# Kernel optimization log

Measured on AMD Instinct MI355X. Metric: run time of the kernel, lower is better.

## Reference

```python
import jax, jax.numpy as jnp
import numpy as np

N_TERMS = 2048  # zonotope error terms (x[0] center + 2047 generators)
N = 4096        # neurons


def setup_inputs() -> dict:
    key = jax.random.key(0)
    x = jax.random.normal(key, (N_TERMS, N), dtype=jnp.float32)
    return {"x": x}


def reference(x):
    n_terms, n = x.shape
    # interval bounds of the zonotope
    abs_sum = jnp.sum(jnp.abs(x[1:]), axis=0)      # [n]
    upper = x[0] + abs_sum
    lower = x[0] - abs_sum

    cross = (lower * upper) < 0                    # neuron straddles 0
    pos = lower >= 0                               # strictly non-negative
    crossf = cross.astype(x.dtype)
    posf = pos.astype(x.dtype)

    # 'auto' lambda init: upper/(upper-lower) on crossing neurons, 1 on positive,
    # NaN (0/0) replaced by 0.5; lambda is set via .data => constant w.r.t. x.
    denom = upper - lower
    safe = denom != 0
    lam = posf + crossf * jnp.where(safe, upper / jnp.where(safe, denom, 1.0), 0.5)
    lam = jax.lax.stop_gradient(lam)

    delta = jnp.maximum(-lam * lower, (1.0 - lam) * upper)  # [n]

    center = (delta * 0.5 + lam * x[0]) * crossf + x[0] * posf
    gens = x[1:] * (lam * crossf + posf)                    # [n_terms-1, n]

    # Parallel stream-compaction: crossing neuron i gets its own new error row
    # at n_terms + (# crossings before i). Padded to worst case n new rows;
    # non-crossing writes land on distinct (row, col) slots with value 0.
    ci = cross.astype(jnp.int32)
    rows = n_terms + jnp.cumsum(ci) - ci               # exclusive prefix sum
    cols = jnp.arange(n)

    out = jnp.zeros((n_terms + n, n), x.dtype)
    out = out.at[0].set(center)
    out = out.at[1:n_terms].set(gens)
    out = out.at[rows, cols].add((delta * 0.5) * crossf)
    return out
```

## Files before the change

### kernel.cpp

```cpp
#include <hip/hip_runtime.h>

#define N_TERMS 2048
#define NCOL 4096
#define NC4 (NCOL / 4)
#define NCHUNK 128
#define ROWS_PER_CHUNK (N_TERMS / NCHUNK)

__global__ void k_partial_abs(const float* __restrict__ x, float* __restrict__ partial) {
    int col4 = blockIdx.x * blockDim.x + threadIdx.x;
    int chunk = blockIdx.y;
    int r0 = chunk * ROWS_PER_CHUNK;
    int r1 = r0 + ROWS_PER_CHUNK;
    if (r0 == 0) r0 = 1;
    const float4* x4 = (const float4*)x;
    float4 acc = {0.f, 0.f, 0.f, 0.f};
#pragma unroll
    for (int r = r0; r < r1; ++r) {
        float4 v = x4[(long)r * NC4 + col4];
        acc.x += fabsf(v.x);
        acc.y += fabsf(v.y);
        acc.z += fabsf(v.z);
        acc.w += fabsf(v.w);
    }
    ((float4*)partial)[chunk * NC4 + col4] = acc;
}

__global__ void k_stats(const float* __restrict__ x, const float* __restrict__ partial,
                        float* __restrict__ out0, float* __restrict__ scale,
                        float* __restrict__ dhalf, int* __restrict__ crossflag) {
    int c = blockIdx.x * blockDim.x + threadIdx.x;
    float s0 = 0.f, s1 = 0.f, s2 = 0.f, s3 = 0.f;
#pragma unroll 4
    for (int k = 0; k < NCHUNK; k += 4) {
        s0 += partial[(k + 0) * NCOL + c];
        s1 += partial[(k + 1) * NCOL + c];
        s2 += partial[(k + 2) * NCOL + c];
        s3 += partial[(k + 3) * NCOL + c];
    }
    float s = (s0 + s1) + (s2 + s3);
    float x0 = x[c];
    float u = x0 + s;
    float l = x0 - s;
    bool cross = (l * u) < 0.0f;
    bool pos = (l >= 0.0f);
    float denom = u - l;
    float lam = (pos ? 1.0f : 0.0f) +
                (cross ? ((denom != 0.0f) ? u / denom : 0.5f) : 0.0f);
    float delta = fmaxf(-lam * l, (1.0f - lam) * u);
    float crossf = cross ? 1.0f : 0.0f;
    float posf = pos ? 1.0f : 0.0f;
    out0[c] = (delta * 0.5f + lam * x0) * crossf + x0 * posf;
    scale[c] = lam * crossf + posf;
    dhalf[c] = delta * 0.5f * crossf;
    crossflag[c] = cross ? 1 : 0;
}

__global__ void k_prefix(const int* __restrict__ crossflag, int* __restrict__ rowtarget) {
    const int T = 256;
    const int PER = NCOL / T;
    __shared__ int tsum[T];
    int t = threadIdx.x;
    int base = t * PER;
    int ex[PER];
    int run = 0;
#pragma unroll
    for (int i = 0; i < PER; ++i) {
        ex[i] = run;
        run += crossflag[base + i];
    }
    tsum[t] = run;
    __syncthreads();
    for (int off = 1; off < T; off <<= 1) {
        int v = 0;
        if (t >= off) v = tsum[t - off];
        __syncthreads();
        tsum[t] += v;
        __syncthreads();
    }
    int excl = (t == 0) ? 0 : tsum[t - 1];
#pragma unroll
    for (int i = 0; i < PER; ++i) rowtarget[base + i] = N_TERMS + excl + ex[i];
}

__global__ void k_write(const float* __restrict__ x, const float* __restrict__ scale,
                        const float* __restrict__ dhalf, const int* __restrict__ rowtarget,
                        float* __restrict__ out) {
    long gidx = (long)blockIdx.x * blockDim.x + threadIdx.x;
    int row = (int)(gidx >> 10) + 1;
    int col4 = (int)(gidx & 1023);
    const float4* x4 = (const float4*)x;
    float4* o4 = (float4*)out;
    if (row < N_TERMS) {
        float4 v = x4[(long)row * NC4 + col4];
        float4 sc = ((const float4*)scale)[col4];
        v.x *= sc.x; v.y *= sc.y; v.z *= sc.z; v.w *= sc.w;
        o4[(long)row * NC4 + col4] = v;
    } else {
        int4 rt = ((const int4*)rowtarget)[col4];
        float4 dh = ((const float4*)dhalf)[col4];
        float4 v;
        v.x = (rt.x == row) ? dh.x : 0.0f;
        v.y = (rt.y == row) ? dh.y : 0.0f;
        v.z = (rt.z == row) ? dh.z : 0.0f;
        v.w = (rt.w == row) ? dh.w : 0.0f;
        o4[(long)row * NC4 + col4] = v;
    }
}

extern "C" void kernel_launch(void* const* d_in, const int* in_sizes, int n_in,
                              void* d_out, int out_size, void* d_ws, size_t ws_size,
                              hipStream_t stream) {
    const float* x = (const float*)d_in[0];
    float* out = (float*)d_out;

    float* ws = (float*)d_ws;
    float* partial   = ws;
    float* scale     = partial + NCHUNK * NCOL;
    float* dhalf     = scale + NCOL;
    int*   crossflag = (int*)(dhalf + NCOL);
    int*   rowtarget = crossflag + NCOL;

    k_partial_abs<<<dim3(NC4 / 256, NCHUNK), 256, 0, stream>>>(x, partial);
    k_stats<<<NCOL / 256, 256, 0, stream>>>(x, partial, out, scale, dhalf, crossflag);
    k_prefix<<<1, 256, 0, stream>>>(crossflag, rowtarget);

    const long total4 = (long)(N_TERMS + NCOL - 1) * NC4;
    const int blocks = (int)((total4 + 255) / 256);
    k_write<<<blocks, 256, 0, stream>>>(x, scale, dhalf, rowtarget, out);
}
```

Measured before the change: 140.6 us.

## Fuse four kernels into one cooperative persistent kernel with grid syncs

Merges the partial abs-sum, stats, prefix-scan and write kernels into one cooperative kernel of 512 blocks, separating the phases with grid-wide syncs instead of separate launches. The goal is to remove the launch gaps between the four kernels. In exchange, the final write phase becomes a grid-stride loop over fewer resident blocks. The stats and prefix phases now leave most blocks idle at a grid barrier, and each grid.sync carries its own cost.

```diff
diff --git a/kernel.cpp b/kernel.cpp
--- a/kernel.cpp
+++ b/kernel.cpp
@@ -1,109 +1,126 @@
 #include <hip/hip_runtime.h>
+#include <hip/hip_cooperative_groups.h>
+
+namespace cg = cooperative_groups;
 
 #define N_TERMS 2048
 #define NCOL 4096
-#define NC4 (NCOL / 4)
+#define NC4 1024
 #define NCHUNK 128
-#define ROWS_PER_CHUNK (N_TERMS / NCHUNK)
+#define RPC (N_TERMS / NCHUNK)
+#define NBLK 512
+#define NTHR 256
 
-__global__ void k_partial_abs(const float* __restrict__ x, float* __restrict__ partial) {
-    int col4 = blockIdx.x * blockDim.x + threadIdx.x;
-    int chunk = blockIdx.y;
-    int r0 = chunk * ROWS_PER_CHUNK;
-    int r1 = r0 + ROWS_PER_CHUNK;
-    if (r0 == 0) r0 = 1;
+__global__ void __launch_bounds__(NTHR, 2)
+k_fused(const float* __restrict__ x, float* __restrict__ out, float* __restrict__ ws) {
+    float* partial   = ws;
+    float* scale     = partial + NCHUNK * NCOL;
+    float* dhalf     = scale + NCOL;
+    int*   crossflag = (int*)(dhalf + NCOL);
+    int*   rowtarget = crossflag + NCOL;
+
+    cg::grid_group grid = cg::this_grid();
+    const int b = blockIdx.x;
+    const int t = threadIdx.x;
     const float4* x4 = (const float4*)x;
-    float4 acc = {0.f, 0.f, 0.f, 0.f};
+
+    {
+        int chunk = b >> 2;
+        int col4  = (b & 3) * NTHR + t;
+        int r0 = chunk * RPC;
+        int r1 = r0 + RPC;
+        if (r0 == 0) r0 = 1;
+        float4 acc = {0.f, 0.f, 0.f, 0.f};
 #pragma unroll
-    for (int r = r0; r < r1; ++r) {
-        float4 v = x4[(long)r * NC4 + col4];
-        acc.x += fabsf(v.x);
-        acc.y += fabsf(v.y);
-        acc.z += fabsf(v.z);
-        acc.w += fabsf(v.w);
+        for (int r = r0; r < r1; ++r) {
+            float4 v = x4[(long)r * NC4 + col4];
+            acc.x += fabsf(v.x);
+            acc.y += fabsf(v.y);
+            acc.z += fabsf(v.z);
+            acc.w += fabsf(v.w);
+        }
+        ((float4*)partial)[chunk * NC4 + col4] = acc;
     }
-    ((float4*)partial)[chunk * NC4 + col4] = acc;
-}
+    __threadfence();
+    grid.sync();
 
-__global__ void k_stats(const float* __restrict__ x, const float* __restrict__ partial,
-                        float* __restrict__ out0, float* __restrict__ scale,
-                        float* __restrict__ dhalf, int* __restrict__ crossflag) {
-    int c = blockIdx.x * blockDim.x + threadIdx.x;
-    float s0 = 0.f, s1 = 0.f, s2 = 0.f, s3 = 0.f;
+    if (b < 16) {
+        int c = b * NTHR + t;
+        float s0 = 0.f, s1 = 0.f, s2 = 0.f, s3 = 0.f;
 #pragma unroll 4
-    for (int k = 0; k < NCHUNK; k += 4) {
-        s0 += partial[(k + 0) * NCOL + c];
-        s1 += partial[(k + 1) * NCOL + c];
-        s2 += partial[(k + 2) * NCOL + c];
-        s3 += partial[(k + 3) * NCOL + c];
+        for (int k = 0; k < NCHUNK; k += 4) {
+            s0 += partial[(k + 0) * NCOL + c];
+            s1 += partial[(k + 1) * NCOL + c];
+            s2 += partial[(k + 2) * NCOL + c];
+            s3 += partial[(k + 3) * NCOL + c];
+        }
+        float s = (s0 + s1) + (s2 + s3);
+        float x0 = x[c];
+        float u = x0 + s;
+        float l = x0 - s;
+        bool cross = (l * u) < 0.0f;
+        bool pos = (l >= 0.0f);
+        float denom = u - l;
+        float lam = (pos ? 1.0f : 0.0f) +
+                    (cross ? ((denom != 0.0f) ? u / denom : 0.5f) : 0.0f);
+        float delta = fmaxf(-lam * l, (1.0f - lam) * u);
+        float crossf = cross ? 1.0f : 0.0f;
+        float posf = pos ? 1.0f : 0.0f;
+        out[c] = (delta * 0.5f + lam * x0) * crossf + x0 * posf;
+        scale[c] = lam * crossf + posf;
+        dhalf[c] = delta * 0.5f * crossf;
+        crossflag[c] = cross ? 1 : 0;
     }
-    float s = (s0 + s1) + (s2 + s3);
-    float x0 = x[c];
-    float u = x0 + s;
-    float l = x0 - s;
-    bool cross = (l * u) < 0.0f;
-    bool pos = (l >= 0.0f);
-    float denom = u - l;
-    float lam = (pos ? 1.0f : 0.0f) +
-                (cross ? ((denom != 0.0f) ? u / denom : 0.5f) : 0.0f);
-    float delta = fmaxf(-lam * l, (1.0f - lam) * u);
-    float crossf = cross ? 1.0f : 0.0f;
-    float posf = pos ? 1.0f : 0.0f;
-    out0[c] = (delta * 0.5f + lam * x0) * crossf + x0 * posf;
-    scale[c] = lam * crossf + posf;
-    dhalf[c] = delta * 0.5f * crossf;
-    crossflag[c] = cross ? 1 : 0;
-}
+    __threadfence();
+    grid.sync();
 
-__global__ void k_prefix(const int* __restrict__ crossflag, int* __restrict__ rowtarget) {
-    const int T = 256;
-    const int PER = NCOL / T;
-    __shared__ int tsum[T];
-    int t = threadIdx.x;
-    int base = t * PER;
-    int ex[PER];
-    int run = 0;
+    __shared__ int tsum[NTHR];
+    if (b == 0) {
+        const int PER = NCOL / NTHR;
+        int base = t * PER;
+        int ex[PER];
+        int run = 0;
 #pragma unroll
-    for (int i = 0; i < PER; ++i) {
-        ex[i] = run;
-        run += crossflag[base + i];
+        for (int i = 0; i < PER; ++i) {
+            ex[i] = run;
+            run += crossflag[base + i];
+        }
+        tsum[t] = run;
+        __syncthreads();
+        for (int off = 1; off < NTHR; off <<= 1) {
+            int v = 0;
+            if (t >= off) v = tsum[t - off];
+            __syncthreads();
+            tsum[t] += v;
+            __syncthreads();
+        }
+        int excl = (t == 0) ? 0 : tsum[t - 1];
+#pragma unroll
+        for (int i = 0; i < PER; ++i) rowtarget[base + i] = N_TERMS + excl + ex[i];
     }
-    tsum[t] = run;
-    __syncthreads();
-    for (int off = 1; off < T; off <<= 1) {
-        int v = 0;
-        if (t >= off) v = tsum[t - off];
-        __syncthreads();
-        tsum[t] += v;
-        __syncthreads();
-    }
-    int excl = (t == 0) ? 0 : tsum[t - 1];
-#pragma unroll
-    for (int i = 0; i < PER; ++i) rowtarget[base + i] = N_TERMS + excl + ex[i];
-}
+    __threadfence();
+    grid.sync();
 
-__global__ void k_write(const float* __restrict__ x, const float* __restrict__ scale,
-                        const float* __restrict__ dhalf, const int* __restrict__ rowtarget,
-                        float* __restrict__ out) {
-    long gidx = (long)blockIdx.x * blockDim.x + threadIdx.x;
-    int row = (int)(gidx >> 10) + 1;
-    int col4 = (int)(gidx & 1023);
-    const float4* x4 = (const float4*)x;
+    const long total4 = (long)(N_TERMS + NCOL - 1) * NC4;
     float4* o4 = (float4*)out;
-    if (row < N_TERMS) {
-        float4 v = x4[(long)row * NC4 + col4];
-        float4 sc = ((const float4*)scale)[col4];
-        v.x *= sc.x; v.y *= sc.y; v.z *= sc.z; v.w *= sc.w;
-        o4[(long)row * NC4 + col4] = v;
-    } else {
-        int4 rt = ((const int4*)rowtarget)[col4];
-        float4 dh = ((const float4*)dhalf)[col4];
-        float4 v;
-        v.x = (rt.x == row) ? dh.x : 0.0f;
-        v.y = (rt.y == row) ? dh.y : 0.0f;
-        v.z = (rt.z == row) ? dh.z : 0.0f;
-        v.w = (rt.w == row) ? dh.w : 0.0f;
-        o4[(long)row * NC4 + col4] = v;
+    for (long g = (long)b * NTHR + t; g < total4; g += (long)NBLK * NTHR) {
+        int row  = (int)(g >> 10) + 1;
+        int col4 = (int)(g & 1023);
+        if (row < N_TERMS) {
+            float4 v = x4[(long)row * NC4 + col4];
+            float4 sc = ((const float4*)scale)[col4];
+            v.x *= sc.x; v.y *= sc.y; v.z *= sc.z; v.w *= sc.w;
+            o4[(long)row * NC4 + col4] = v;
+        } else {
+            int4 rt = ((const int4*)rowtarget)[col4];
+            float4 dh = ((const float4*)dhalf)[col4];
+            float4 v;
+            v.x = (rt.x == row) ? dh.x : 0.0f;
+            v.y = (rt.y == row) ? dh.y : 0.0f;
+            v.z = (rt.z == row) ? dh.z : 0.0f;
+            v.w = (rt.w == row) ? dh.w : 0.0f;
+            o4[(long)row * NC4 + col4] = v;
+        }
     }
 }
 
@@ -112,19 +129,9 @@
                               hipStream_t stream) {
     const float* x = (const float*)d_in[0];
     float* out = (float*)d_out;
+    float* ws = (float*)d_ws;
 
-    float* ws = (float*)d_ws;
-    float* partial   = ws;
-    float* scale     = partial + NCHUNK * NCOL;
-    float* dhalf     = scale + NCOL;
-    int*   crossflag = (int*)(dhalf + NCOL);
-    int*   rowtarget = crossflag + NCOL;
-
-    k_partial_abs<<<dim3(NC4 / 256, NCHUNK), 256, 0, stream>>>(x, partial);
-    k_stats<<<NCOL / 256, 256, 0, stream>>>(x, partial, out, scale, dhalf, crossflag);
-    k_prefix<<<1, 256, 0, stream>>>(crossflag, rowtarget);
-
-    const long total4 = (long)(N_TERMS + NCOL - 1) * NC4;
-    const int blocks = (int)((total4 + 255) / 256);
-    k_write<<<blocks, 256, 0, stream>>>(x, scale, dhalf, rowtarget, out);
+    void* args[] = {(void*)&x, (void*)&out, (void*)&ws};
+    hipLaunchCooperativeKernel((const void*)k_fused, dim3(NBLK), dim3(NTHR),
+                               args, 0, stream);
 }
```

Result: slower. 411.3 us (+192.5%).
